# Optimization experiments

Hardware: AMD Instinct MI355X
Metric: run time of the kernel (lower is better)

## Reference

```python
import jax, jax.numpy as jnp
import numpy as np
from jax import lax

N_T, B, C_IN, H, W = 24, 2, 9, 32, 32   # n timesteps, batch, bands, tile HxW
N_FILTER, KM, N_CLASS, HID = 32, 16, 10, 128


def setup_inputs() -> dict:
    key = jax.random.key(0)
    ks = jax.random.split(key, 6)
    x = jax.random.normal(ks[0], (N_T, B, C_IN, H, W), jnp.float32)
    kernels = jax.random.normal(ks[1], (N_FILTER, KM, C_IN), jnp.float32)  # DTW filter kernels
    W1 = jax.random.normal(ks[2], (N_FILTER, HID), jnp.float32) * 0.1
    b1 = jnp.zeros((HID,), jnp.float32)
    W2 = jax.random.normal(ks[3], (HID, HID), jnp.float32) * 0.1
    b2 = jnp.zeros((HID,), jnp.float32)
    Wl = jax.random.normal(ks[4], (HID, N_CLASS), jnp.float32) * 0.1
    bl = jnp.zeros((N_CLASS,), jnp.float32)
    return {"x": x, "kernels": kernels, "W1": W1, "b1": b1, "W2": W2, "b2": b2, "Wl": Wl, "bl": bl}


def _dtw_single(kernel, seq):
    # kernel: (m, c), seq: (n, c). Classic DTW with squared-euclidean local cost,
    # then sum of local costs along the optimal alignment path (path is non-diff,
    # matching the torch code's detached dtw_path + differentiable squared diffs).
    C = jnp.sum((kernel[:, None, :] - seq[None, :, :]) ** 2, axis=-1)  # (m, n)
    m, n = C.shape
    inf = jnp.array(jnp.inf, C.dtype)
    row0 = jnp.cumsum(C[0])

    def row_step(prev, crow):
        prev_shift = jnp.concatenate([jnp.full((1,), inf, C.dtype), prev[:-1]])
        def col_step(left, cud):
            c, up, diag = cud
            d = c + jnp.minimum(left, jnp.minimum(up, diag))
            return d, d
        _, row = lax.scan(col_step, inf, (crow, prev, prev_shift))
        return row, row

    _, rows = lax.scan(row_step, row0, C[1:])
    D = lax.stop_gradient(jnp.concatenate([row0[None, :], rows], axis=0))  # (m, n)

    def bt_step(carry, _):
        i, j, acc, done = carry
        im1 = jnp.maximum(i - 1, 0)
        jm1 = jnp.maximum(j - 1, 0)
        cand = jnp.stack([
            jnp.where((i > 0) & (j > 0), D[im1, jm1], inf),  # diagonal
            jnp.where(i > 0, D[im1, j], inf),                # up
            jnp.where(j > 0, D[i, jm1], inf)])               # left
        choice = jnp.argmin(cand)  # first-min tie-break = diagonal preferred (as np.argmin)
        ni = jnp.where(choice == 2, i, im1)
        nj = jnp.where(choice == 1, j, jm1)
        ni = jnp.where(done, i, ni)
        nj = jnp.where(done, j, nj)
        acc = acc + jnp.where(done, jnp.array(0.0, C.dtype), C[ni, nj])
        done = done | ((ni == 0) & (nj == 0))
        return (ni, nj, acc, done), None

    init = (jnp.int32(m - 1), jnp.int32(n - 1), C[m - 1, n - 1], jnp.array(m == 1 and n == 1))
    (_, _, total, _), _ = lax.scan(bt_step, init, None, length=m + n - 2)
    return total


def reference(x, kernels, W1, b1, W2, b2, Wl, bl):
    n, b, c, h, w = x.shape
    # torch.cat(list_of_n, dim=0).view(-1, n, c) == row-major reshape of (n,b,c,h,w)
    seqs = x.reshape(-1, n, c)  # (B2, n, c), B2 = b*h*w
    feats = jax.vmap(lambda s: jax.vmap(lambda k: _dtw_single(k, s))(kernels))(seqs)  # (B2, F)
    t = jax.nn.relu(feats @ W1 + b1)
    t = jax.nn.relu(t @ W2 + b2)
    t = jax.nn.softmax(t @ Wl + bl, axis=1)
    return t.reshape(b, N_CLASS, h, w)
```

## Files before the change

kernel.cpp:

```cpp
#include <hip/hip_runtime.h>

#define NT   24
#define CIN  9
#define NF   32
#define KM   16
#define HID  128
#define NCLS 10
#define SEQ_LEN (NT*CIN)
#define PADJ 12
#define NSTRIP 4

__global__ __launch_bounds__(128, 4) void dtwnet_fused(
    const float* __restrict__ x,
    const float* __restrict__ kern,
    const float* __restrict__ W1, const float* __restrict__ b1,
    const float* __restrict__ W2, const float* __restrict__ b2,
    const float* __restrict__ Wl, const float* __restrict__ bl,
    float* __restrict__ out)
{
  __shared__ float seq_lds[NT*PADJ];
  __shared__ float feat_lds[NF];
  __shared__ float h1_lds[HID];
  __shared__ float h2_lds[HID];
  __shared__ float logit_lds[NCLS];

  const int tid  = threadIdx.x;
  const int bid  = blockIdx.x;
  const int wave = tid >> 6;
  const int lane = tid & 63;
  const int s    = lane >> 4;
  const int f_lo = lane & 15;
  const int f    = wave*16 + f_lo;

  float kf[4*CIN];
  {
    const float4* kp = (const float4*)(kern + f*(KM*CIN) + s*(4*CIN));
    float4 t0 = kp[0], t1 = kp[1], t2 = kp[2], t3 = kp[3], t4 = kp[4],
           t5 = kp[5], t6 = kp[6], t7 = kp[7], t8 = kp[8];
    kf[0]=t0.x; kf[1]=t0.y; kf[2]=t0.z; kf[3]=t0.w;
    kf[4]=t1.x; kf[5]=t1.y; kf[6]=t1.z; kf[7]=t1.w;
    kf[8]=t2.x; kf[9]=t2.y; kf[10]=t2.z; kf[11]=t2.w;
    kf[12]=t3.x; kf[13]=t3.y; kf[14]=t3.z; kf[15]=t3.w;
    kf[16]=t4.x; kf[17]=t4.y; kf[18]=t4.z; kf[19]=t4.w;
    kf[20]=t5.x; kf[21]=t5.y; kf[22]=t5.z; kf[23]=t5.w;
    kf[24]=t6.x; kf[25]=t6.y; kf[26]=t6.z; kf[27]=t6.w;
    kf[28]=t7.x; kf[29]=t7.y; kf[30]=t7.z; kf[31]=t7.w;
    kf[32]=t8.x; kf[33]=t8.y; kf[34]=t8.z; kf[35]=t8.w;
  }

  for (int d = tid; d < SEQ_LEN; d += 128) {
    int jj = d / CIN, cc = d - jj*CIN;
    seq_lds[jj*PADJ + cc] = x[bid*SEQ_LEN + d];
  }
  __syncthreads();

  float rowD[4];
  float bndUp = 0.f, bndDg = 0.f;

  #pragma unroll 1
  for (int t = 0; t < NT + NSTRIP - 1; ++t) {
    int j = t - s;
    bool active = (j >= 0) && (j < NT);
    float nb = 0.f;
    if (active) {
      const float4* sp = (const float4*)(seq_lds + j*PADJ);
      float4 q0 = sp[0], q1 = sp[1], q2 = sp[2];
      float sv[CIN] = {q0.x,q0.y,q0.z,q0.w,q1.x,q1.y,q1.z,q1.w,q2.x};
      float cost[4];
      #pragma unroll
      for (int r = 0; r < 4; ++r) {
        float cc = 0.f;
        #pragma unroll
        for (int c = 0; c < CIN; ++c) { float d = kf[r*CIN+c] - sv[c]; cc = fmaf(d, d, cc); }
        cost[r] = cc;
      }
      if (j == 0) {
        float acc = (s == 0) ? 0.f : bndUp;
        #pragma unroll
        for (int r = 0; r < 4; ++r) { acc += cost[r]; rowD[r] = acc; }
      } else {
        float up, diag;
        float left = rowD[0];
        float D0;
        if (s == 0) {
          D0 = cost[0] + left;
        } else {
          D0 = cost[0] + fminf(bndDg, fminf(bndUp, left));
        }
        diag = left;
        rowD[0] = D0; up = D0;
        #pragma unroll
        for (int r = 1; r < 4; ++r) {
          float lD = rowD[r];
          float D2 = cost[r] + fminf(diag, fminf(up, lD));
          diag = lD;
          rowD[r] = D2; up = D2;
        }
      }
      nb = rowD[3];
    }
    float rD = __shfl_up(nb, 16u);
    bndDg = bndUp;
    bndUp = rD;
  }

  if (s == 3) feat_lds[f] = rowD[3];
  __syncthreads();

  {
    float acc = b1[tid];
    #pragma unroll
    for (int k = 0; k < NF; ++k) acc = fmaf(feat_lds[k], W1[k*HID + tid], acc);
    h1_lds[tid] = fmaxf(acc, 0.f);
  }
  __syncthreads();
  {
    const float4* hh = (const float4*)h1_lds;
    float a0 = b2[tid], a1 = 0.f, a2 = 0.f, a3 = 0.f;
    #pragma unroll
    for (int k = 0; k < HID/4; ++k) {
      float4 h4 = hh[k];
      a0 = fmaf(h4.x, W2[(4*k+0)*HID + tid], a0);
      a1 = fmaf(h4.y, W2[(4*k+1)*HID + tid], a1);
      a2 = fmaf(h4.z, W2[(4*k+2)*HID + tid], a2);
      a3 = fmaf(h4.w, W2[(4*k+3)*HID + tid], a3);
    }
    h2_lds[tid] = fmaxf((a0 + a1) + (a2 + a3), 0.f);
  }
  __syncthreads();
  if (tid < NCLS) {
    const float4* hh = (const float4*)h2_lds;
    float a0 = bl[tid], a1 = 0.f, a2 = 0.f, a3 = 0.f;
    #pragma unroll
    for (int k = 0; k < HID/4; ++k) {
      float4 h4 = hh[k];
      a0 = fmaf(h4.x, Wl[(4*k+0)*NCLS + tid], a0);
      a1 = fmaf(h4.y, Wl[(4*k+1)*NCLS + tid], a1);
      a2 = fmaf(h4.z, Wl[(4*k+2)*NCLS + tid], a2);
      a3 = fmaf(h4.w, Wl[(4*k+3)*NCLS + tid], a3);
    }
    logit_lds[tid] = (a0 + a1) + (a2 + a3);
  }
  __syncthreads();
  if (tid == 0) {
    float mx = logit_lds[0];
    #pragma unroll
    for (int j = 1; j < NCLS; ++j) mx = fmaxf(mx, logit_lds[j]);
    float e[NCLS]; float sum = 0.f;
    #pragma unroll
    for (int j = 0; j < NCLS; ++j) { e[j] = __expf(logit_lds[j] - mx); sum += e[j]; }
    float inv = 1.f / sum;
    float* op = out + bid*NCLS;
    #pragma unroll
    for (int j = 0; j < NCLS; ++j) op[j] = e[j] * inv;
  }
}

extern "C" void kernel_launch(void* const* d_in, const int* in_sizes, int n_in,
                              void* d_out, int out_size, void* d_ws, size_t ws_size,
                              hipStream_t stream) {
  const float* x    = (const float*)d_in[0];
  const float* kern = (const float*)d_in[1];
  const float* W1   = (const float*)d_in[2];
  const float* b1   = (const float*)d_in[3];
  const float* W2   = (const float*)d_in[4];
  const float* b2   = (const float*)d_in[5];
  const float* Wl   = (const float*)d_in[6];
  const float* bl   = (const float*)d_in[7];
  float* out = (float*)d_out;

  dtwnet_fused<<<2048, 128, 0, stream>>>(x, kern, W1, b1, W2, b2, Wl, bl, out);
}
```

Baseline: 86.95 us.

## Expand squared distance algebraically, use packed FMA, process two sequences per block

```diff
diff --git a/kernel.cpp b/kernel.cpp
--- a/kernel.cpp
+++ b/kernel.cpp
@@ -10,7 +10,9 @@
 #define PADJ 12
 #define NSTRIP 4
 
-__global__ __launch_bounds__(128, 4) void dtwnet_fused(
+typedef float vf2 __attribute__((ext_vector_type(2)));
+
+__global__ __launch_bounds__(256, 4) void dtwnet_fused(
     const float* __restrict__ x,
     const float* __restrict__ kern,
     const float* __restrict__ W1, const float* __restrict__ b1,
@@ -18,41 +20,71 @@
     const float* __restrict__ Wl, const float* __restrict__ bl,
     float* __restrict__ out)
 {
-  __shared__ float seq_lds[NT*PADJ];
-  __shared__ float feat_lds[NF];
-  __shared__ float h1_lds[HID];
-  __shared__ float h2_lds[HID];
-  __shared__ float logit_lds[NCLS];
+  __shared__ float seq_lds[2*NT*PADJ];
+  __shared__ float bcol[2*32];
+  __shared__ float feat_lds[2*NF];
+  __shared__ float h1_lds[2*HID];
+  __shared__ float h2_lds[2*HID];
+  __shared__ float logit_lds[2*NCLS];
 
   const int tid  = threadIdx.x;
   const int bid  = blockIdx.x;
   const int wave = tid >> 6;
   const int lane = tid & 63;
+  const int seqi = wave >> 1;
   const int s    = lane >> 4;
   const int f_lo = lane & 15;
-  const int f    = wave*16 + f_lo;
-
-  float kf[4*CIN];
+  const int f    = (wave & 1)*16 + f_lo;
+
+  float kraw[4*CIN];
   {
     const float4* kp = (const float4*)(kern + f*(KM*CIN) + s*(4*CIN));
-    float4 t0 = kp[0], t1 = kp[1], t2 = kp[2], t3 = kp[3], t4 = kp[4],
-           t5 = kp[5], t6 = kp[6], t7 = kp[7], t8 = kp[8];
-    kf[0]=t0.x; kf[1]=t0.y; kf[2]=t0.z; kf[3]=t0.w;
-    kf[4]=t1.x; kf[5]=t1.y; kf[6]=t1.z; kf[7]=t1.w;
-    kf[8]=t2.x; kf[9]=t2.y; kf[10]=t2.z; kf[11]=t2.w;
-    kf[12]=t3.x; kf[13]=t3.y; kf[14]=t3.z; kf[15]=t3.w;
-    kf[16]=t4.x; kf[17]=t4.y; kf[18]=t4.z; kf[19]=t4.w;
-    kf[20]=t5.x; kf[21]=t5.y; kf[22]=t5.z; kf[23]=t5.w;
-    kf[24]=t6.x; kf[25]=t6.y; kf[26]=t6.z; kf[27]=t6.w;
-    kf[28]=t7.x; kf[29]=t7.y; kf[30]=t7.z; kf[31]=t7.w;
-    kf[32]=t8.x; kf[33]=t8.y; kf[34]=t8.z; kf[35]=t8.w;
-  }
-
-  for (int d = tid; d < SEQ_LEN; d += 128) {
-    int jj = d / CIN, cc = d - jj*CIN;
-    seq_lds[jj*PADJ + cc] = x[bid*SEQ_LEN + d];
-  }
-  __syncthreads();
+    float4 t0=kp[0], t1=kp[1], t2=kp[2], t3=kp[3], t4=kp[4],
+           t5=kp[5], t6=kp[6], t7=kp[7], t8=kp[8];
+    kraw[0]=t0.x; kraw[1]=t0.y; kraw[2]=t0.z; kraw[3]=t0.w;
+    kraw[4]=t1.x; kraw[5]=t1.y; kraw[6]=t1.z; kraw[7]=t1.w;
+    kraw[8]=t2.x; kraw[9]=t2.y; kraw[10]=t2.z; kraw[11]=t2.w;
+    kraw[12]=t3.x; kraw[13]=t3.y; kraw[14]=t3.z; kraw[15]=t3.w;
+    kraw[16]=t4.x; kraw[17]=t4.y; kraw[18]=t4.z; kraw[19]=t4.w;
+    kraw[20]=t5.x; kraw[21]=t5.y; kraw[22]=t5.z; kraw[23]=t5.w;
+    kraw[24]=t6.x; kraw[25]=t6.y; kraw[26]=t6.z; kraw[27]=t6.w;
+    kraw[28]=t7.x; kraw[29]=t7.y; kraw[30]=t7.z; kraw[31]=t7.w;
+    kraw[32]=t8.x; kraw[33]=t8.y; kraw[34]=t8.z; kraw[35]=t8.w;
+  }
+
+  for (int d = tid; d < 2*SEQ_LEN; d += 256) {
+    int sq = d / SEQ_LEN;
+    int r  = d - sq*SEQ_LEN;
+    int jj = r / CIN, cc = r - jj*CIN;
+    seq_lds[sq*NT*PADJ + jj*PADJ + cc] = x[bid*(2*SEQ_LEN) + d];
+  }
+  __syncthreads();
+
+  {
+    int sq = tid >> 5, j = tid & 31;
+    if (sq < 2 && j < NT) {
+      const float4* sp = (const float4*)(seq_lds + sq*NT*PADJ + j*PADJ);
+      float4 q0 = sp[0], q1 = sp[1], q2 = sp[2];
+      bcol[sq*32 + j] = q0.x*q0.x + q0.y*q0.y + q0.z*q0.z + q0.w*q0.w
+                      + q1.x*q1.x + q1.y*q1.y + q1.z*q1.z + q1.w*q1.w
+                      + q2.x*q2.x;
+    }
+  }
+
+  vf2 kf01[CIN], kf23[CIN], ar01 = {0.f,0.f}, ar23 = {0.f,0.f};
+  #pragma unroll
+  for (int c = 0; c < CIN; ++c) {
+    vf2 a = {kraw[c],        kraw[CIN+c]};
+    vf2 b = {kraw[2*CIN+c],  kraw[3*CIN+c]};
+    ar01 = __builtin_elementwise_fma(a, a, ar01);
+    ar23 = __builtin_elementwise_fma(b, b, ar23);
+    kf01[c] = a * (-2.f);
+    kf23[c] = b * (-2.f);
+  }
+  __syncthreads();
+
+  const float* sl = seq_lds + seqi*NT*PADJ;
+  const float* bc = bcol + seqi*32;
 
   float rowD[4];
   float bndUp = 0.f, bndDg = 0.f;
@@ -63,23 +95,24 @@
     bool active = (j >= 0) && (j < NT);
     float nb = 0.f;
     if (active) {
-      const float4* sp = (const float4*)(seq_lds + j*PADJ);
+      const float4* sp = (const float4*)(sl + j*PADJ);
       float4 q0 = sp[0], q1 = sp[1], q2 = sp[2];
+      float bj = bc[j];
       float sv[CIN] = {q0.x,q0.y,q0.z,q0.w,q1.x,q1.y,q1.z,q1.w,q2.x};
-      float cost[4];
+      vf2 c01 = ar01 + bj;
+      vf2 c23 = ar23 + bj;
       #pragma unroll
-      for (int r = 0; r < 4; ++r) {
-        float cc = 0.f;
-        #pragma unroll
-        for (int c = 0; c < CIN; ++c) { float d = kf[r*CIN+c] - sv[c]; cc = fmaf(d, d, cc); }
-        cost[r] = cc;
+      for (int c = 0; c < CIN; ++c) {
+        vf2 sc = {sv[c], sv[c]};
+        c01 = __builtin_elementwise_fma(kf01[c], sc, c01);
+        c23 = __builtin_elementwise_fma(kf23[c], sc, c23);
       }
+      float cost[4] = {c01.x, c01.y, c23.x, c23.y};
       if (j == 0) {
         float acc = (s == 0) ? 0.f : bndUp;
         #pragma unroll
         for (int r = 0; r < 4; ++r) { acc += cost[r]; rowD[r] = acc; }
       } else {
-        float up, diag;
         float left = rowD[0];
         float D0;
         if (s == 0) {
@@ -87,8 +120,8 @@
         } else {
           D0 = cost[0] + fminf(bndDg, fminf(bndUp, left));
         }
-        diag = left;
-        rowD[0] = D0; up = D0;
+        float diag = left, up = D0;
+        rowD[0] = D0;
         #pragma unroll
         for (int r = 1; r < 4; ++r) {
           float lD = rowD[r];
@@ -104,53 +137,75 @@
     bndUp = rD;
   }
 
-  if (s == 3) feat_lds[f] = rowD[3];
-  __syncthreads();
-
-  {
-    float acc = b1[tid];
-    #pragma unroll
-    for (int k = 0; k < NF; ++k) acc = fmaf(feat_lds[k], W1[k*HID + tid], acc);
-    h1_lds[tid] = fmaxf(acc, 0.f);
-  }
-  __syncthreads();
-  {
-    const float4* hh = (const float4*)h1_lds;
-    float a0 = b2[tid], a1 = 0.f, a2 = 0.f, a3 = 0.f;
+  if (s == NSTRIP-1) feat_lds[seqi*NF + f] = rowD[3];
+  __syncthreads();
+
+  if (tid < HID) {
+    const float* f0 = feat_lds;
+    const float* f1 = feat_lds + NF;
+    float a0 = b1[tid], a1 = a0;
+    #pragma unroll
+    for (int k = 0; k < NF; ++k) {
+      float w = W1[k*HID + tid];
+      a0 = fmaf(f0[k], w, a0);
+      a1 = fmaf(f1[k], w, a1);
+    }
+    h1_lds[tid]       = fmaxf(a0, 0.f);
+    h1_lds[HID + tid] = fmaxf(a1, 0.f);
+  }
+  __syncthreads();
+  if (tid < HID) {
+    const float4* h0 = (const float4*)h1_lds;
+    const float4* h1v = (const float4*)(h1_lds + HID);
+    float p0 = b2[tid], p1 = 0.f, p2 = 0.f, p3 = 0.f;
+    float q0 = b2[tid], q1 = 0.f, q2 = 0.f, q3 = 0.f;
     #pragma unroll
     for (int k = 0; k < HID/4; ++k) {
-      float4 h4 = hh[k];
-      a0 = fmaf(h4.x, W2[(4*k+0)*HID + tid], a0);
-      a1 = fmaf(h4.y, W2[(4*k+1)*HID + tid], a1);
-      a2 = fmaf(h4.z, W2[(4*k+2)*HID + tid], a2);
-      a3 = fmaf(h4.w, W2[(4*k+3)*HID + tid], a3);
-    }
-    h2_lds[tid] = fmaxf((a0 + a1) + (a2 + a3), 0.f);
+      float w0 = W2[(4*k+0)*HID + tid];
+      float w1 = W2[(4*k+1)*HID + tid];
+      float w2 = W2[(4*k+2)*HID + tid];
+      float w3 = W2[(4*k+3)*HID + tid];
+      float4 ha = h0[k], hb = h1v[k];
+      p0 = fmaf(ha.x, w0, p0); p1 = fmaf(ha.y, w1, p1);
+      p2 = fmaf(ha.z, w2, p2); p3 = fmaf(ha.w, w3, p3);
+      q0 = fmaf(hb.x, w0, q0); q1 = fmaf(hb.y, w1, q1);
+      q2 = fmaf(hb.z, w2, q2); q3 = fmaf(hb.w, w3, q3);
+    }
+    h2_lds[tid]       = fmaxf((p0 + p1) + (p2 + p3), 0.f);
+    h2_lds[HID + tid] = fmaxf((q0 + q1) + (q2 + q3), 0.f);
   }
   __syncthreads();
   if (tid < NCLS) {
-    const float4* hh = (const float4*)h2_lds;
-    float a0 = bl[tid], a1 = 0.f, a2 = 0.f, a3 = 0.f;
+    const float4* h0 = (const float4*)h2_lds;
+    const float4* h1v = (const float4*)(h2_lds + HID);
+    float p0 = bl[tid], p1 = 0.f, p2 = 0.f, p3 = 0.f;
+    float q0 = bl[tid], q1 = 0.f, q2 = 0.f, q3 = 0.f;
     #pragma unroll
     for (int k = 0; k < HID/4; ++k) {
-      float4 h4 = hh[k];
-      a0 = fmaf(h4.x, Wl[(4*k+0)*NCLS + tid], a0);
-      a1 = fmaf(h4.y, Wl[(4*k+1)*NCLS + tid], a1);
-      a2 = fmaf(h4.z, Wl[(4*k+2)*NCLS + tid], a2);
-      a3 = fmaf(h4.w, Wl[(4*k+3)*NCLS + tid], a3);
-    }
-    logit_lds[tid] = (a0 + a1) + (a2 + a3);
-  }
-  __syncthreads();
-  if (tid == 0) {
-    float mx = logit_lds[0];
-    #pragma unroll
-    for (int j = 1; j < NCLS; ++j) mx = fmaxf(mx, logit_lds[j]);
+      float w0 = Wl[(4*k+0)*NCLS + tid];
+      float w1 = Wl[(4*k+1)*NCLS + tid];
+      float w2 = Wl[(4*k+2)*NCLS + tid];
+      float w3 = Wl[(4*k+3)*NCLS + tid];
+      float4 ha = h0[k], hb = h1v[k];
+      p0 = fmaf(ha.x, w0, p0); p1 = fmaf(ha.y, w1, p1);
+      p2 = fmaf(ha.z, w2, p2); p3 = fmaf(ha.w, w3, p3);
+      q0 = fmaf(hb.x, w0, q0); q1 = fmaf(hb.y, w1, q1);
+      q2 = fmaf(hb.z, w2, q2); q3 = fmaf(hb.w, w3, q3);
+    }
+    logit_lds[tid]        = (p0 + p1) + (p2 + p3);
+    logit_lds[NCLS + tid] = (q0 + q1) + (q2 + q3);
+  }
+  __syncthreads();
+  if (tid < 2) {
+    const float* lg = &logit_lds[tid*NCLS];
+    float mx = lg[0];
+    #pragma unroll
+    for (int j = 1; j < NCLS; ++j) mx = fmaxf(mx, lg[j]);
     float e[NCLS]; float sum = 0.f;
     #pragma unroll
-    for (int j = 0; j < NCLS; ++j) { e[j] = __expf(logit_lds[j] - mx); sum += e[j]; }
+    for (int j = 0; j < NCLS; ++j) { e[j] = __expf(lg[j] - mx); sum += e[j]; }
     float inv = 1.f / sum;
-    float* op = out + bid*NCLS;
+    float* op = out + (bid*2 + tid)*NCLS;
     #pragma unroll
     for (int j = 0; j < NCLS; ++j) op[j] = e[j] * inv;
   }
@@ -169,5 +224,5 @@
   const float* bl   = (const float*)d_in[7];
   float* out = (float*)d_out;
 
-  dtwnet_fused<<<2048, 128, 0, stream>>>(x, kern, W1, b1, W2, b2, Wl, bl, out);
+  dtwnet_fused<<<1024, 256, 0, stream>>>(x, kern, W1, b1, W2, b2, Wl, bl, out);
 }
```

Result: faster. 84.92 us (-2.3%).
